# Kernel optimization log

Measured on AMD Instinct MI355X. Metric: run time of the kernel, lower is better.

Reference implementation:

```python
import jax, jax.numpy as jnp
import numpy as np

N_NODES = 50000
N_EDGES = 800000
IN_DIM = 128
OUT_DIM = 128
NUM_EDGE_TYPES = 16
RULE_FEAT_DIM = 4


def setup_inputs() -> dict:
    key = jax.random.key(0)
    ks = jax.random.split(key, 20)
    d = OUT_DIM
    s_in = 1.0 / np.sqrt(IN_DIM)
    s_d = 1.0 / np.sqrt(d)
    s_r = 1.0 / np.sqrt(RULE_FEAT_DIM)
    inp = {
        "x": jax.random.normal(ks[0], (N_NODES, IN_DIM), jnp.float32),
        "edge_index": jax.random.randint(ks[1], (2, N_EDGES), 0, N_NODES),
        "edge_type": jax.random.randint(ks[2], (N_EDGES,), 0, NUM_EDGE_TYPES),
        "edge_rule_feat": jax.random.normal(ks[3], (N_EDGES, RULE_FEAT_DIM), jnp.float32),
        "total_nodes": N_NODES,
        # parameters (Linear stored as [in, out]; y = x @ W + b)
        "Wq": jax.random.uniform(ks[4], (IN_DIM, d), jnp.float32, -s_in, s_in),
        "bq": jnp.zeros((d,), jnp.float32),
        "Wk": jax.random.uniform(ks[5], (IN_DIM, d), jnp.float32, -s_in, s_in),
        "bk": jnp.zeros((d,), jnp.float32),
        "Wv": jax.random.uniform(ks[6], (IN_DIM, d), jnp.float32, -s_in, s_in),
        "bv": jnp.zeros((d,), jnp.float32),
        "rel_emb": jax.random.normal(ks[7], (NUM_EDGE_TYPES, d), jnp.float32),
        "attn_vec": jax.random.normal(ks[8], (3 * d,), jnp.float32),
        "rule_w1": jax.random.uniform(ks[9], (RULE_FEAT_DIM, d), jnp.float32, -s_r, s_r),
        "rule_b1": jnp.zeros((d,), jnp.float32),
        "rule_w2": jax.random.uniform(ks[10], (d, 1), jnp.float32, -s_d, s_d),
        "rule_b2": jnp.zeros((1,), jnp.float32),  # zero-initialized in source
        "gate_rule_w": jax.random.uniform(ks[11], (RULE_FEAT_DIM, 1), jnp.float32, -s_r, s_r),
        "gate_rule_b": jnp.zeros((1,), jnp.float32),
        "gate_neural_w": jax.random.uniform(ks[12], (2 * d, 1), jnp.float32, -1.0 / np.sqrt(2 * d), 1.0 / np.sqrt(2 * d)),
        "gate_neural_b": jnp.zeros((1,), jnp.float32),
        "msg_w": jax.random.uniform(ks[13], (d, d), jnp.float32, -s_d, s_d),
        "msg_b": jnp.zeros((d,), jnp.float32),
    }
    return inp


def reference(x, edge_index, edge_type, edge_rule_feat, total_nodes,
              Wq, bq, Wk, bk, Wv, bv, rel_emb, attn_vec,
              rule_w1, rule_b1, rule_w2, rule_b2,
              gate_rule_w, gate_rule_b, gate_neural_w, gate_neural_b,
              msg_w, msg_b):
    src, dst = edge_index[0], edge_index[1]
    d = msg_w.shape[0]

    h_src = x[src] @ Wk + bk                  # [E, d]
    h_dst = x[dst] @ Wq + bq                  # [E, d]
    rel = rel_emb[edge_type]                  # [E, d]

    # (cat([h_src,h_dst,rel]) * attn_vec).sum(-1) without materializing the concat
    a1, a2, a3 = attn_vec[:d], attn_vec[d:2 * d], attn_vec[2 * d:]
    e_base = jax.nn.leaky_relu(h_src @ a1 + h_dst @ a2 + rel @ a3, negative_slope=0.2)

    hidden = jax.nn.relu(edge_rule_feat @ rule_w1 + rule_b1)
    b_ij = (hidden @ rule_w2)[:, 0] + rule_b2[0]          # rule bias per edge

    gate_logit = (edge_rule_feat @ gate_rule_w)[:, 0] + gate_rule_b[0] \
               + (h_src @ gate_neural_w[:d, 0] + h_dst @ gate_neural_w[d:, 0]) + gate_neural_b[0]
    gamma_ij = jax.nn.sigmoid(gate_logit)

    e = e_base + gamma_ij * b_ij

    n = total_nodes
    # segment softmax over dst (numerically stable)
    seg_max = jax.ops.segment_max(e, dst, num_segments=n)
    e_exp = jnp.exp(e - seg_max[dst])
    seg_sum = jax.ops.segment_sum(e_exp, dst, num_segments=n)
    alpha = e_exp / (seg_sum[dst] + 1e-16)

    # eval mode: dropout is identity
    msg = ((x[src] @ Wv + bv + rel) @ msg_w + msg_b) * alpha[:, None]
    out = jax.ops.segment_sum(msg, dst, num_segments=n)   # index_add over dst
    return out, alpha, gamma_ij, b_ij
```

## Files before the change

kernel.cpp:

```cpp
#include <hip/hip_runtime.h>
#include <math.h>


using bf16x8 = __attribute__((ext_vector_type(8))) short;
using f32x4  = __attribute__((ext_vector_type(4))) float;

__device__ __forceinline__ float wave_max(float v) {
    #pragma unroll
    for (int o = 32; o > 0; o >>= 1) v = fmaxf(v, __shfl_xor(v, o, 64));
    return v;
}
__device__ __forceinline__ float wave_sum(float v) {
    #pragma unroll
    for (int o = 32; o > 0; o >>= 1) v += __shfl_xor(v, o, 64);
    return v;
}

__device__ __forceinline__ unsigned bf16rne(float f) {
    unsigned u = __float_as_uint(f);
    return (u + 0x7FFFu + ((u >> 16) & 1u)) >> 16;
}
__device__ __forceinline__ float bflo(unsigned u) { return __uint_as_float(u << 16); }
__device__ __forceinline__ float bfhi(unsigned u) { return __uint_as_float(u & 0xFFFF0000u); }

__global__ void __launch_bounds__(128) precompute_kernel(
    const float* __restrict__ Wq, const float* __restrict__ bq,
    const float* __restrict__ Wk, const float* __restrict__ bk,
    const float* __restrict__ Wv, const float* __restrict__ bv,
    const float* __restrict__ rel_emb, const float* __restrict__ attn_vec,
    const float* __restrict__ msg_w, const float* __restrict__ msg_b,
    const float* __restrict__ gnw, const float* __restrict__ grb,
    const float* __restrict__ gnb,
    const float* __restrict__ rule_w1, const float* __restrict__ rule_b1,
    const float* __restrict__ rule_w2,
    unsigned short* __restrict__ W2bT, float* __restrict__ c2,
    float* __restrict__ wkA, float* __restrict__ wqA,
    float* __restrict__ wkG, float* __restrict__ wqG,
    float* __restrict__ relA, float* __restrict__ relM,
    float* __restrict__ consts,
    float4* __restrict__ w1t, float2* __restrict__ w12)
{
    __shared__ float red[128];
    int bid = blockIdx.x, j = threadIdx.x;

    auto blk_reduce = [&](float v) -> float {
        red[j] = v;
        __syncthreads();
        for (int s = 64; s > 0; s >>= 1) {
            if (j < s) red[j] += red[j + s];
            __syncthreads();
        }
        float r = red[0];
        __syncthreads();
        return r;
    };

    if (bid < 128) {
        int i = bid;
        float acc = 0.f;
        #pragma unroll 8
        for (int k = 0; k < 128; ++k) acc = fmaf(Wv[i * 128 + k], msg_w[k * 128 + j], acc);
        W2bT[j * 128 + i] = (unsigned short)bf16rne(acc);
        float r;
        r = blk_reduce(Wk[i * 128 + j] * attn_vec[j]);        if (j == 0) wkA[i] = r;
        r = blk_reduce(Wq[i * 128 + j] * attn_vec[128 + j]);  if (j == 0) wqA[i] = r;
        r = blk_reduce(Wk[i * 128 + j] * gnw[j]);             if (j == 0) wkG[i] = r;
        r = blk_reduce(Wq[i * 128 + j] * gnw[128 + j]);       if (j == 0) wqG[i] = r;
    } else if (bid < 144) {
        int t = bid - 128;
        float acc = 0.f;
        #pragma unroll 8
        for (int k = 0; k < 128; ++k) acc = fmaf(rel_emb[t * 128 + k], msg_w[k * 128 + j], acc);
        relM[t * 128 + j] = acc;
        float r = blk_reduce(rel_emb[t * 128 + j] * attn_vec[256 + j]);
        if (j == 0) relA[t] = r;
    } else if (bid == 144) {
        float acc = msg_b[j];
        #pragma unroll 8
        for (int k = 0; k < 128; ++k) acc = fmaf(bv[k], msg_w[k * 128 + j], acc);
        c2[j] = acc;
        w1t[j] = make_float4(rule_w1[j], rule_w1[128 + j], rule_w1[256 + j], rule_w1[384 + j]);
        w12[j] = make_float2(rule_b1[j], rule_w2[j]);
    } else {
        float r = blk_reduce(bk[j] * attn_vec[j] + bq[j] * attn_vec[128 + j]);
        if (j == 0) consts[0] = r;
        r = blk_reduce(bk[j] * gnw[j] + bq[j] * gnw[128 + j]);
        if (j == 0) consts[1] = r + grb[0] + gnb[0];
    }
}

__global__ void __launch_bounds__(256) node_kernel(
    const float4* __restrict__ x4, const unsigned short* __restrict__ W2bT,
    const float* __restrict__ c2,
    const float* __restrict__ wkA, const float* __restrict__ wqA,
    const float* __restrict__ wkG, const float* __restrict__ wqG,
    unsigned* __restrict__ Vmb, float2* __restrict__ srcPack,
    float2* __restrict__ dstPack, int n_nodes)
{
    __shared__ unsigned short Asu[128][136];
    __shared__ unsigned short Bsu[128][136];
    const int tid = threadIdx.x;
    const int rowBase = blockIdx.x * 128;

    #pragma unroll
    for (int l = 0; l < 16; ++l) {
        int flat = l * 256 + tid;
        int r = flat >> 5, k4 = flat & 31;
        int row = rowBase + r;
        float4 v = (row < n_nodes) ? x4[row * 32 + k4] : make_float4(0.f, 0.f, 0.f, 0.f);
        uint2 u;
        u.x = bf16rne(v.x) | (bf16rne(v.y) << 16);
        u.y = bf16rne(v.z) | (bf16rne(v.w) << 16);
        *(uint2*)&Asu[r][k4 * 4] = u;
    }
    #pragma unroll
    for (int l = 0; l < 16; ++l) {
        int flat = l * 256 + tid;
        int n = flat >> 5, kq = flat & 31;
        uint2 w = *(const uint2*)&W2bT[n * 128 + kq * 4];
        *(uint2*)&Bsu[n][kq * 4] = w;
    }

    {
        int r = tid & 127, h = tid >> 7;
        int row = rowBase + r;
        if (row < n_nodes) {
            const float4* wa4 = (const float4*)(h ? wqA : wkA);
            const float4* wg4 = (const float4*)(h ? wqG : wkG);
            float sA = 0.f, sG = 0.f;
            #pragma unroll 8
            for (int k4 = 0; k4 < 32; ++k4) {
                float4 xv = x4[row * 32 + k4];
                float4 wa = wa4[k4], wg = wg4[k4];
                sA = fmaf(xv.x, wa.x, fmaf(xv.y, wa.y, fmaf(xv.z, wa.z, fmaf(xv.w, wa.w, sA))));
                sG = fmaf(xv.x, wg.x, fmaf(xv.y, wg.y, fmaf(xv.z, wg.z, fmaf(xv.w, wg.w, sG))));
            }
            if (h) dstPack[row] = make_float2(sA, sG);
            else   srcPack[row] = make_float2(sA, sG);
        }
    }
    __syncthreads();

    const int wave = tid >> 6, lane = tid & 63;
    const int ln = lane & 15, quad = lane >> 4;
    const int wm = (wave & 1) * 64, wn = (wave >> 1) * 64;

    f32x4 acc[4][4];
    #pragma unroll
    for (int i = 0; i < 4; ++i)
        #pragma unroll
        for (int j = 0; j < 4; ++j) acc[i][j] = (f32x4){0.f, 0.f, 0.f, 0.f};

    #pragma unroll
    for (int kc = 0; kc < 4; ++kc) {
        int k0 = kc * 32 + quad * 8;
        bf16x8 afr[4], bfr[4];
        #pragma unroll
        for (int mt = 0; mt < 4; ++mt)
            afr[mt] = *(const bf16x8*)&Asu[wm + mt * 16 + ln][k0];
        #pragma unroll
        for (int nt = 0; nt < 4; ++nt)
            bfr[nt] = *(const bf16x8*)&Bsu[wn + nt * 16 + ln][k0];
        #pragma unroll
        for (int mt = 0; mt < 4; ++mt)
            #pragma unroll
            for (int nt = 0; nt < 4; ++nt)
                acc[mt][nt] = __builtin_amdgcn_mfma_f32_16x16x32_bf16(
                    afr[mt], bfr[nt], acc[mt][nt], 0, 0, 0);
    }

    #pragma unroll
    for (int nt = 0; nt < 4; ++nt) {
        int col = wn + nt * 16 + ln;
        float cb = c2[col];
        #pragma unroll
        for (int mt = 0; mt < 4; ++mt) {
            #pragma unroll
            for (int r = 0; r < 4; ++r) {
                int row = rowBase + wm + mt * 16 + quad * 4 + r;
                float v = acc[mt][nt][r] + cb;
                float pv = __shfl_xor(v, 1, 64);
                if (!(ln & 1) && row < n_nodes) {
                    Vmb[row * 64 + (col >> 1)] = bf16rne(v) | (bf16rne(pv) << 16);
                }
            }
        }
    }
}

__global__ void __launch_bounds__(256) edge1a_kernel(
    const float4* __restrict__ erf,
    const float4* __restrict__ w1t, const float2* __restrict__ w12,
    const float* __restrict__ rule_b2,
    float* __restrict__ b_out, int n_edges)
{
    __shared__ float4 s_w1t[128];
    __shared__ float2 s_w12[128];
    const int tid = threadIdx.x;
    if (tid < 128) { s_w1t[tid] = w1t[tid]; s_w12[tid] = w12[tid]; }
    __syncthreads();

    const int eb = blockIdx.x * 1024;
    float4 rf[4];
    #pragma unroll
    for (int q = 0; q < 4; ++q) {
        int e = eb + q * 256 + tid;
        rf[q] = erf[min(e, n_edges - 1)];
    }

    float bacc[4] = {0.f, 0.f, 0.f, 0.f};
    #pragma unroll 2
    for (int j = 0; j < 128; ++j) {
        float4 w = s_w1t[j];
        float2 c = s_w12[j];
        #pragma unroll
        for (int q = 0; q < 4; ++q) {
            float h = fmaf(rf[q].x, w.x, fmaf(rf[q].y, w.y,
                      fmaf(rf[q].z, w.z, fmaf(rf[q].w, w.w, c.x))));
            bacc[q] = fmaf(fmaxf(h, 0.f), c.y, bacc[q]);
        }
    }

    const float rb2 = rule_b2[0];
    #pragma unroll
    for (int q = 0; q < 4; ++q) {
        int e = eb + q * 256 + tid;
        if (e < n_edges) b_out[e] = bacc[q] + rb2;
    }
}

__global__ void __launch_bounds__(256) edge1b_kernel(
    const int* __restrict__ ei, const int* __restrict__ et,
    const float4* __restrict__ erf, const float* __restrict__ grw,
    const float2* __restrict__ srcPack, const float2* __restrict__ dstPack,
    const float* __restrict__ relA, const float* __restrict__ consts,
    const float* __restrict__ b_out,
    float* __restrict__ e_val, float* __restrict__ gamma_out,
    int n_edges)
{
    int e = blockIdx.x * 256 + threadIdx.x;
    if (e >= n_edges) return;

    int s = ei[e], d = ei[n_edges + e], t = et[e];
    float4 rf = erf[e];
    float b = b_out[e];
    float2 ss = srcPack[s], dd = dstPack[d];

    float pre = ss.x + dd.x + relA[t] + consts[0];
    float e_base = pre >= 0.f ? pre : 0.2f * pre;

    float gl = fmaf(rf.x, grw[0], fmaf(rf.y, grw[1],
               fmaf(rf.z, grw[2], fmaf(rf.w, grw[3], consts[1] + ss.y + dd.y))));
    float gamma = 1.f / (1.f + __expf(-gl));

    gamma_out[e] = gamma;
    e_val[e] = e_base + gamma * b;
}

__global__ void __launch_bounds__(256) histo_kernel(
    const int* __restrict__ dsts, int* __restrict__ hpart, int n_edges)
{
    __shared__ int cnt[256];
    const int tid = threadIdx.x;
    cnt[tid] = 0;
    __syncthreads();
    const int base = blockIdx.x * 4096;
    const int end = min(base + 4096, n_edges);
    for (int e = base + tid; e < end; e += 256)
        atomicAdd(&cnt[dsts[e] >> 8], 1);
    __syncthreads();
    hpart[blockIdx.x * 256 + tid] = cnt[tid];
}

__global__ void __launch_bounds__(256) hscan_kernel(
    const int* __restrict__ hpart, int* __restrict__ bucketCursor,
    int* __restrict__ bucketStart, int* __restrict__ rowPtr,
    int nblk, int n_nodes, int n_edges)
{
    __shared__ int sdata[256];
    const int tid = threadIdx.x;
    int s = 0;
    for (int i = 0; i < nblk; ++i) s += hpart[i * 256 + tid];
    sdata[tid] = s;
    __syncthreads();
    #pragma unroll
    for (int off = 1; off < 256; off <<= 1) {
        int t = (tid >= off) ? sdata[tid - off] : 0;
        __syncthreads();
        sdata[tid] += t;
        __syncthreads();
    }
    int excl = sdata[tid] - s;
    bucketCursor[tid] = excl;
    bucketStart[tid] = excl;
    if (tid == 0) rowPtr[n_nodes] = n_edges;
}

__global__ void __launch_bounds__(256) sort1_kernel(
    const int* __restrict__ ei, const int* __restrict__ et,
    const float* __restrict__ e_val, int* __restrict__ bucketCursor,
    float2* __restrict__ tmp, int n_edges)
{
    __shared__ float2 data[4096];
    __shared__ unsigned char slotB[4096];
    __shared__ int cnt[256], rk[256], base_[256], run[256], scanBuf[256];
    const int tid = threadIdx.x;
    const int blockBase = blockIdx.x * 4096;
    const int total = min(4096, n_edges - blockBase);

    cnt[tid] = 0;
    rk[tid] = 0;
    __syncthreads();

    int   d_[16];
    float ev_[16];
    int   pk_[16];
    #pragma unroll
    for (int i = 0; i < 16; ++i) {
        int e = blockBase + i * 256 + tid;
        if (e < n_edges) {
            int d = ei[n_edges + e];
            d_[i]  = d;
            ev_[i] = e_val[e];
            pk_[i] = (ei[e] & 0xFFFF) | ((et[e] & 15) << 16) | ((d & 255) << 20);
            atomicAdd(&cnt[d >> 8], 1);
        } else {
            d_[i] = -1;
        }
    }
    __syncthreads();

    int c = cnt[tid];
    scanBuf[tid] = c;
    __syncthreads();
    #pragma unroll
    for (int off = 1; off < 256; off <<= 1) {
        int t = (tid >= off) ? scanBuf[tid - off] : 0;
        __syncthreads();
        scanBuf[tid] += t;
        __syncthreads();
    }
    base_[tid] = scanBuf[tid] - c;
    run[tid] = c ? atomicAdd(&bucketCursor[tid], c) : 0;
    __syncthreads();

    #pragma unroll
    for (int i = 0; i < 16; ++i) {
        if (d_[i] >= 0) {
            int b = d_[i] >> 8;
            int r = atomicAdd(&rk[b], 1);
            int slot = base_[b] + r;
            data[slot] = make_float2(ev_[i], __int_as_float(pk_[i]));
            slotB[slot] = (unsigned char)b;
        }
    }
    __syncthreads();

    for (int j = tid; j < total; j += 256) {
        int b = slotB[j];
        tmp[run[b] + (j - base_[b])] = data[j];
    }
}

__global__ void __launch_bounds__(256) sort2_kernel(
    const int* __restrict__ bucketStart, const float2* __restrict__ tmp,
    float2* __restrict__ payload, int* __restrict__ rowPtr,
    int n_nodes, int n_edges, int nbuck)
{
    __shared__ int cnt[256], cur[256], sdata[256];
    const int tid = threadIdx.x;
    const int b = blockIdx.x;
    const int d0 = b * 256;
    const int lo = bucketStart[b];
    const int hi = (b == nbuck - 1) ? n_edges : bucketStart[b + 1];

    cnt[tid] = 0;
    __syncthreads();
    for (int j = lo + tid; j < hi; j += 256) {
        unsigned pk = __float_as_uint(tmp[j].y);
        atomicAdd(&cnt[(pk >> 20) & 255], 1);
    }
    __syncthreads();

    int c = cnt[tid];
    sdata[tid] = c;
    __syncthreads();
    #pragma unroll
    for (int off = 1; off < 256; off <<= 1) {
        int t = (tid >= off) ? sdata[tid - off] : 0;
        __syncthreads();
        sdata[tid] += t;
        __syncthreads();
    }
    int excl = sdata[tid] - c;
    cur[tid] = lo + excl;
    if (d0 + tid < n_nodes) rowPtr[d0 + tid] = lo + excl;
    __syncthreads();

    for (int j = lo + tid; j < hi; j += 256) {
        float2 p = tmp[j];
        unsigned pk = __float_as_uint(p.y);
        int dl = (pk >> 20) & 255;
        int pos = atomicAdd(&cur[dl], 1);
        unsigned st = (pk & 0xFFFFu) | (((pk >> 16) & 15u) << 27);
        payload[pos] = make_float2(p.x, __uint_as_float(st));
    }
}

__global__ void __launch_bounds__(256) gather_kernel(
    const int* __restrict__ rowPtr, const float2* __restrict__ payload,
    const unsigned* __restrict__ Vmb, const float* __restrict__ relM,
    float* __restrict__ out, float2* __restrict__ nodeMS, int n_nodes)
{
    __shared__ float2 s_relM[16 * 64];
    const int tid = threadIdx.x;
    const float2* relM2 = (const float2*)relM;
    #pragma unroll
    for (int i = 0; i < 4; ++i) s_relM[i * 256 + tid] = relM2[i * 256 + tid];
    __syncthreads();

    int lane = tid & 63;
    int d = blockIdx.x * 4 + (tid >> 6);
    if (d >= n_nodes) return;
    int start = rowPtr[d];
    int deg = rowPtr[d + 1] - start;

    float acc0 = 0.f, acc1 = 0.f;
    float m = -INFINITY, inv;

    auto acc8 = [&](float av, int st, int k) {
        float a[8];
        int s[8];
        #pragma unroll
        for (int i = 0; i < 8; ++i) {
            a[i] = __shfl(av, k + i, 64);
            s[i] = __shfl(st, k + i, 64);
        }
        unsigned v[8];
        float2 rm[8];
        #pragma unroll
        for (int i = 0; i < 8; ++i) {
            int ss = s[i] & 0x7FFFFFF;
            int tt = ((unsigned)s[i]) >> 27;
            v[i]  = Vmb[ss * 64 + lane];
            rm[i] = s_relM[tt * 64 + lane];
        }
        #pragma unroll
        for (int i = 0; i < 8; ++i) {
            acc0 = fmaf(a[i], bflo(v[i]) + rm[i].x, acc0);
            acc1 = fmaf(a[i], bfhi(v[i]) + rm[i].y, acc1);
        }
    };

    if (deg <= 64) {
        float ev = -INFINITY;
        int st = 0;
        if (lane < deg) {
            float2 p = payload[start + lane];
            ev = p.x;
            st = __float_as_int(p.y);
        }
        m = wave_max(ev);
        float ex = (lane < deg) ? __expf(ev - m) : 0.f;
        float sum = wave_sum(ex);
        inv = 1.f / (sum + 1e-16f);
        float av = ex * inv;
        for (int k = 0; k < deg; k += 8) acc8(av, st, k);
    } else {
        for (int i = lane; i < deg; i += 64) m = fmaxf(m, payload[start + i].x);
        m = wave_max(m);
        float sum = 0.f;
        for (int i = lane; i < deg; i += 64) sum += __expf(payload[start + i].x - m);
        sum = wave_sum(sum);
        inv = 1.f / (sum + 1e-16f);
        for (int c = 0; c < deg; c += 64) {
            int i = c + lane;
            float av = 0.f;
            int st = 0;
            if (i < deg) {
                float2 p = payload[start + i];
                av = __expf(p.x - m) * inv;
                st = __float_as_int(p.y);
            }
            int cnt = min(64, deg - c);
            for (int k = 0; k < cnt; k += 8) acc8(av, st, k);
        }
    }
    if (lane == 0) nodeMS[d] = make_float2(m, inv);
    *(float2*)&out[d * 128 + lane * 2] = make_float2(acc0, acc1);
}

__global__ void __launch_bounds__(256) alpha_kernel(
    const int* __restrict__ ei, const float* __restrict__ e_val,
    const float2* __restrict__ nodeMS, float* __restrict__ alpha_out, int n_edges)
{
    int e = blockIdx.x * blockDim.x + threadIdx.x;
    if (e >= n_edges) return;
    int d = ei[n_edges + e];
    float2 ms = nodeMS[d];
    alpha_out[e] = __expf(e_val[e] - ms.x) * ms.y;
}

extern "C" void kernel_launch(void* const* d_in, const int* in_sizes, int n_in,
                              void* d_out, int out_size, void* d_ws, size_t ws_size,
                              hipStream_t stream)
{
    const float* x        = (const float*)d_in[0];
    const int*   ei       = (const int*)d_in[1];
    const int*   et       = (const int*)d_in[2];
    const float* erf      = (const float*)d_in[3];
    const float* Wq       = (const float*)d_in[5];
    const float* bq       = (const float*)d_in[6];
    const float* Wk       = (const float*)d_in[7];
    const float* bk       = (const float*)d_in[8];
    const float* Wv       = (const float*)d_in[9];
    const float* bv       = (const float*)d_in[10];
    const float* rel_emb  = (const float*)d_in[11];
    const float* attn_vec = (const float*)d_in[12];
    const float* rule_w1  = (const float*)d_in[13];
    const float* rule_b1  = (const float*)d_in[14];
    const float* rule_w2  = (const float*)d_in[15];
    const float* rule_b2  = (const float*)d_in[16];
    const float* grw      = (const float*)d_in[17];
    const float* grb      = (const float*)d_in[18];
    const float* gnw      = (const float*)d_in[19];
    const float* gnb      = (const float*)d_in[20];
    const float* msg_w    = (const float*)d_in[21];
    const float* msg_b    = (const float*)d_in[22];

    const int n_nodes = in_sizes[0] / 128;
    const int n_edges = in_sizes[2];
    const int nhb = (n_edges + 4095) / 4096;
    const int nbuck = (n_nodes + 255) / 256;

    float* ws = (float*)d_ws;
    size_t off = 0;
    unsigned* Vmb  = (unsigned*)(ws + off); off += (size_t)n_nodes * 64;
    float2* payload = (float2*)(ws + off); off += 2 * (size_t)n_edges;
    float2* tmpPay  = (float2*)(ws + off); off += 2 * (size_t)n_edges;
    float* e_val   = ws + off; off += n_edges;
    float* srcPack = ws + off; off += 2 * (size_t)n_nodes;
    float* dstPack = ws + off; off += 2 * (size_t)n_nodes;
    float2* nodeMS = (float2*)(ws + off); off += 2 * (size_t)n_nodes;
    int*   rowPtr  = (int*)(ws + off); off += n_nodes + 4;
    int*   hpart   = (int*)(ws + off); off += (size_t)nhb * 256;
    int*   bucketCursor = (int*)(ws + off); off += 256;
    int*   bucketStart  = (int*)(ws + off); off += 256;
    unsigned short* W2bT = (unsigned short*)(ws + off); off += 128 * 64;
    float* c2      = ws + off; off += 128;
    float* wkA     = ws + off; off += 128;
    float* wqA     = ws + off; off += 128;
    float* wkG     = ws + off; off += 128;
    float* wqG     = ws + off; off += 128;
    float* relA    = ws + off; off += 16;
    float* relM    = ws + off; off += 16 * 128;
    float* consts  = ws + off; off += 2;
    off += 2;
    float4* w1t    = (float4*)(ws + off); off += 128 * 4;
    float2* w12    = (float2*)(ws + off); off += 128 * 2;

    float* out       = (float*)d_out;
    float* alpha_out = out + (size_t)n_nodes * 128;
    float* gamma_out = alpha_out + n_edges;
    float* b_out     = gamma_out + n_edges;

    hipLaunchKernelGGL(precompute_kernel, dim3(146), dim3(128), 0, stream,
                       Wq, bq, Wk, bk, Wv, bv, rel_emb, attn_vec, msg_w, msg_b,
                       gnw, grb, gnb, rule_w1, rule_b1, rule_w2,
                       W2bT, c2, wkA, wqA, wkG, wqG, relA, relM, consts, w1t, w12);

    hipLaunchKernelGGL(histo_kernel, dim3(nhb), dim3(256), 0, stream,
                       ei + n_edges, hpart, n_edges);

    hipLaunchKernelGGL(hscan_kernel, dim3(1), dim3(256), 0, stream,
                       hpart, bucketCursor, bucketStart, rowPtr,
                       nhb, n_nodes, n_edges);

    hipLaunchKernelGGL(node_kernel, dim3((n_nodes + 127) / 128), dim3(256), 0, stream,
                       (const float4*)x, W2bT, c2,
                       wkA, wqA, wkG, wqG, Vmb, (float2*)srcPack, (float2*)dstPack,
                       n_nodes);

    hipLaunchKernelGGL(edge1a_kernel, dim3((n_edges + 1023) / 1024), dim3(256), 0, stream,
                       (const float4*)erf, (const float4*)w1t, (const float2*)w12,
                       rule_b2, b_out, n_edges);

    hipLaunchKernelGGL(edge1b_kernel, dim3((n_edges + 255) / 256), dim3(256), 0, stream,
                       ei, et, (const float4*)erf, grw,
                       (const float2*)srcPack, (const float2*)dstPack,
                       relA, consts, b_out, e_val, gamma_out, n_edges);

    hipLaunchKernelGGL(sort1_kernel, dim3(nhb), dim3(256), 0, stream,
                       ei, et, e_val, bucketCursor, tmpPay, n_edges);

    hipLaunchKernelGGL(sort2_kernel, dim3(nbuck), dim3(256), 0, stream,
                       bucketStart, tmpPay, payload, rowPtr,
                       n_nodes, n_edges, nbuck);

    hipLaunchKernelGGL(gather_kernel, dim3((n_nodes + 3) / 4), dim3(256), 0, stream,
                       rowPtr, payload, Vmb, relM, out, nodeMS, n_nodes);

    hipLaunchKernelGGL(alpha_kernel, dim3((n_edges + 255) / 256), dim3(256), 0, stream,
                       ei, e_val, nodeMS, alpha_out, n_edges);
}
```

Measured before the change: 295.8 us.

## Fuse histogram into rule-MLP kernel and edge scoring into bucket sort

Moves the destination histogram count into edge1a_kernel, which now handles 2048 edges per block and writes per-block partial counts. Folds the former edge1b scoring (leaky-relu attention, gate sigmoid, e_val and gamma) into sort1_kernel, so e_val is computed in registers rather than written and read back. Two kernels and their launches go away, along with a pass over the edge index and e_val. In exchange edge1a uses more registers per thread, sort1 does more work per thread with random srcPack/dstPack gathers, and hscan now scans more, smaller partial histograms.

```diff
diff --git a/kernel.cpp b/kernel.cpp
--- a/kernel.cpp
+++ b/kernel.cpp
@@ -189,32 +189,35 @@
 }
 
 __global__ void __launch_bounds__(256) edge1a_kernel(
-    const float4* __restrict__ erf,
+    const float4* __restrict__ erf, const int* __restrict__ dsts,
     const float4* __restrict__ w1t, const float2* __restrict__ w12,
     const float* __restrict__ rule_b2,
-    float* __restrict__ b_out, int n_edges)
+    float* __restrict__ b_out, int* __restrict__ hpart, int n_edges)
 {
     __shared__ float4 s_w1t[128];
     __shared__ float2 s_w12[128];
+    __shared__ int cnt[256];
     const int tid = threadIdx.x;
     if (tid < 128) { s_w1t[tid] = w1t[tid]; s_w12[tid] = w12[tid]; }
-    __syncthreads();
-
-    const int eb = blockIdx.x * 1024;
-    float4 rf[4];
-    #pragma unroll
-    for (int q = 0; q < 4; ++q) {
+    cnt[tid] = 0;
+    __syncthreads();
+
+    const int eb = blockIdx.x * 2048;
+    float4 rf[8];
+    #pragma unroll
+    for (int q = 0; q < 8; ++q) {
         int e = eb + q * 256 + tid;
         rf[q] = erf[min(e, n_edges - 1)];
-    }
-
-    float bacc[4] = {0.f, 0.f, 0.f, 0.f};
+        if (e < n_edges) atomicAdd(&cnt[dsts[e] >> 8], 1);
+    }
+
+    float bacc[8] = {0.f, 0.f, 0.f, 0.f, 0.f, 0.f, 0.f, 0.f};
     #pragma unroll 2
     for (int j = 0; j < 128; ++j) {
         float4 w = s_w1t[j];
         float2 c = s_w12[j];
         #pragma unroll
-        for (int q = 0; q < 4; ++q) {
+        for (int q = 0; q < 8; ++q) {
             float h = fmaf(rf[q].x, w.x, fmaf(rf[q].y, w.y,
                       fmaf(rf[q].z, w.z, fmaf(rf[q].w, w.w, c.x))));
             bacc[q] = fmaf(fmaxf(h, 0.f), c.y, bacc[q]);
@@ -223,51 +226,10 @@
 
     const float rb2 = rule_b2[0];
     #pragma unroll
-    for (int q = 0; q < 4; ++q) {
+    for (int q = 0; q < 8; ++q) {
         int e = eb + q * 256 + tid;
         if (e < n_edges) b_out[e] = bacc[q] + rb2;
     }
-}
-
-__global__ void __launch_bounds__(256) edge1b_kernel(
-    const int* __restrict__ ei, const int* __restrict__ et,
-    const float4* __restrict__ erf, const float* __restrict__ grw,
-    const float2* __restrict__ srcPack, const float2* __restrict__ dstPack,
-    const float* __restrict__ relA, const float* __restrict__ consts,
-    const float* __restrict__ b_out,
-    float* __restrict__ e_val, float* __restrict__ gamma_out,
-    int n_edges)
-{
-    int e = blockIdx.x * 256 + threadIdx.x;
-    if (e >= n_edges) return;
-
-    int s = ei[e], d = ei[n_edges + e], t = et[e];
-    float4 rf = erf[e];
-    float b = b_out[e];
-    float2 ss = srcPack[s], dd = dstPack[d];
-
-    float pre = ss.x + dd.x + relA[t] + consts[0];
-    float e_base = pre >= 0.f ? pre : 0.2f * pre;
-
-    float gl = fmaf(rf.x, grw[0], fmaf(rf.y, grw[1],
-               fmaf(rf.z, grw[2], fmaf(rf.w, grw[3], consts[1] + ss.y + dd.y))));
-    float gamma = 1.f / (1.f + __expf(-gl));
-
-    gamma_out[e] = gamma;
-    e_val[e] = e_base + gamma * b;
-}
-
-__global__ void __launch_bounds__(256) histo_kernel(
-    const int* __restrict__ dsts, int* __restrict__ hpart, int n_edges)
-{
-    __shared__ int cnt[256];
-    const int tid = threadIdx.x;
-    cnt[tid] = 0;
-    __syncthreads();
-    const int base = blockIdx.x * 4096;
-    const int end = min(base + 4096, n_edges);
-    for (int e = base + tid; e < end; e += 256)
-        atomicAdd(&cnt[dsts[e] >> 8], 1);
     __syncthreads();
     hpart[blockIdx.x * 256 + tid] = cnt[tid];
 }
@@ -298,19 +260,28 @@
 
 __global__ void __launch_bounds__(256) sort1_kernel(
     const int* __restrict__ ei, const int* __restrict__ et,
-    const float* __restrict__ e_val, int* __restrict__ bucketCursor,
-    float2* __restrict__ tmp, int n_edges)
+    const float4* __restrict__ erf, const float* __restrict__ b_out,
+    const float* __restrict__ grw,
+    const float2* __restrict__ srcPack, const float2* __restrict__ dstPack,
+    const float* __restrict__ relA, const float* __restrict__ consts,
+    float* __restrict__ e_val, float* __restrict__ gamma_out,
+    int* __restrict__ bucketCursor, float2* __restrict__ tmp, int n_edges)
 {
     __shared__ float2 data[4096];
     __shared__ unsigned char slotB[4096];
     __shared__ int cnt[256], rk[256], base_[256], run[256], scanBuf[256];
+    __shared__ float s_relA[16];
     const int tid = threadIdx.x;
     const int blockBase = blockIdx.x * 4096;
     const int total = min(4096, n_edges - blockBase);
 
     cnt[tid] = 0;
     rk[tid] = 0;
-    __syncthreads();
+    if (tid < 16) s_relA[tid] = relA[tid];
+    __syncthreads();
+
+    const float c0 = consts[0], c1 = consts[1];
+    const float g0 = grw[0], g1 = grw[1], g2 = grw[2], g3 = grw[3];
 
     int   d_[16];
     float ev_[16];
@@ -319,10 +290,23 @@
     for (int i = 0; i < 16; ++i) {
         int e = blockBase + i * 256 + tid;
         if (e < n_edges) {
+            int s = ei[e];
             int d = ei[n_edges + e];
+            int t = et[e];
+            float4 rf = erf[e];
+            float b = b_out[e];
+            float2 ss = srcPack[s], dd = dstPack[d];
+            float pre = ss.x + dd.x + s_relA[t] + c0;
+            float e_base = pre >= 0.f ? pre : 0.2f * pre;
+            float gl = fmaf(rf.x, g0, fmaf(rf.y, g1,
+                       fmaf(rf.z, g2, fmaf(rf.w, g3, c1 + ss.y + dd.y))));
+            float gamma = 1.f / (1.f + __expf(-gl));
+            float ev = e_base + gamma * b;
+            gamma_out[e] = gamma;
+            e_val[e] = ev;
             d_[i]  = d;
-            ev_[i] = e_val[e];
-            pk_[i] = (ei[e] & 0xFFFF) | ((et[e] & 15) << 16) | ((d & 255) << 20);
+            ev_[i] = ev;
+            pk_[i] = (s & 0xFFFF) | ((t & 15) << 16) | ((d & 255) << 20);
             atomicAdd(&cnt[d >> 8], 1);
         } else {
             d_[i] = -1;
@@ -530,6 +514,7 @@
 
     const int n_nodes = in_sizes[0] / 128;
     const int n_edges = in_sizes[2];
+    const int nab = (n_edges + 2047) / 2048;
     const int nhb = (n_edges + 4095) / 4096;
     const int nbuck = (n_nodes + 255) / 256;
 
@@ -543,7 +528,7 @@
     float* dstPack = ws + off; off += 2 * (size_t)n_nodes;
     float2* nodeMS = (float2*)(ws + off); off += 2 * (size_t)n_nodes;
     int*   rowPtr  = (int*)(ws + off); off += n_nodes + 4;
-    int*   hpart   = (int*)(ws + off); off += (size_t)nhb * 256;
+    int*   hpart   = (int*)(ws + off); off += (size_t)nab * 256;
     int*   bucketCursor = (int*)(ws + off); off += 256;
     int*   bucketStart  = (int*)(ws + off); off += 256;
     unsigned short* W2bT = (unsigned short*)(ws + off); off += 128 * 64;
@@ -569,29 +554,25 @@
                        gnw, grb, gnb, rule_w1, rule_b1, rule_w2,
                        W2bT, c2, wkA, wqA, wkG, wqG, relA, relM, consts, w1t, w12);
 
-    hipLaunchKernelGGL(histo_kernel, dim3(nhb), dim3(256), 0, stream,
-                       ei + n_edges, hpart, n_edges);
-
-    hipLaunchKernelGGL(hscan_kernel, dim3(1), dim3(256), 0, stream,
-                       hpart, bucketCursor, bucketStart, rowPtr,
-                       nhb, n_nodes, n_edges);
-
     hipLaunchKernelGGL(node_kernel, dim3((n_nodes + 127) / 128), dim3(256), 0, stream,
                        (const float4*)x, W2bT, c2,
                        wkA, wqA, wkG, wqG, Vmb, (float2*)srcPack, (float2*)dstPack,
                        n_nodes);
 
-    hipLaunchKernelGGL(edge1a_kernel, dim3((n_edges + 1023) / 1024), dim3(256), 0, stream,
-                       (const float4*)erf, (const float4*)w1t, (const float2*)w12,
-                       rule_b2, b_out, n_edges);
-
-    hipLaunchKernelGGL(edge1b_kernel, dim3((n_edges + 255) / 256), dim3(256), 0, stream,
-                       ei, et, (const float4*)erf, grw,
+    hipLaunchKernelGGL(edge1a_kernel, dim3(nab), dim3(256), 0, stream,
+                       (const float4*)erf, ei + n_edges,
+                       (const float4*)w1t, (const float2*)w12,
+                       rule_b2, b_out, hpart, n_edges);
+
+    hipLaunchKernelGGL(hscan_kernel, dim3(1), dim3(256), 0, stream,
+                       hpart, bucketCursor, bucketStart, rowPtr,
+                       nab, n_nodes, n_edges);
+
+    hipLaunchKernelGGL(sort1_kernel, dim3(nhb), dim3(256), 0, stream,
+                       ei, et, (const float4*)erf, b_out, grw,
                        (const float2*)srcPack, (const float2*)dstPack,
-                       relA, consts, b_out, e_val, gamma_out, n_edges);
-
-    hipLaunchKernelGGL(sort1_kernel, dim3(nhb), dim3(256), 0, stream,
-                       ei, et, e_val, bucketCursor, tmpPay, n_edges);
+                       relA, consts, e_val, gamma_out,
+                       bucketCursor, tmpPay, n_edges);
 
     hipLaunchKernelGGL(sort2_kernel, dim3(nbuck), dim3(256), 0, stream,
                        bucketStart, tmpPay, payload, rowPtr,
```

New measurement: 321.3 us. 1.09x slower.
